# Performance work log

Measured on AMD Instinct MI355X. Metric: run time of the kernel, lower is better.

## Reference

```python
import jax, jax.numpy as jnp
import numpy as np


def setup_inputs() -> dict:
    key = jax.random.key(0)
    kq, kk, kv = jax.random.split(key, 3)
    B, M, QT, KVT, H = 2, 16, 2048, 2048, 128
    q = jax.random.normal(kq, (B, M, QT, H), dtype=jnp.float32)
    k = jax.random.normal(kk, (B, M, KVT, H), dtype=jnp.float32)
    v = jax.random.normal(kv, (B, M, KVT, H), dtype=jnp.float32)
    return {"q": q, "k": k, "v": v}


def reference(q, k, v):
    # QKBmm: broadcast-multiply + sum == einsum contraction over H.
    # NOTE: original module applies NO 1/sqrt(H) scaling.
    score = jnp.einsum("bmqh,bmkh->bmqk", q, k)  # [B,M,QT,KVT]
    score = jax.nn.softmax(score, axis=-1)
    # SVBmm: broadcast-multiply + sum over KVT.
    out = jnp.einsum("bmqk,bmkh->bmqh", score, v)  # [B,M,QT,H]
    return out
```

## Files before the change

### kernel.cpp

```cpp
#include <hip/hip_runtime.h>
#include <hip/hip_bf16.h>
#include <math.h>


#define HD     128
#define QTL    2048
#define KVTL   2048
#define NHEAD  32
#define KVBLK  64
#define NKT    (KVTL / KVBLK)
#define QBLKB  128
#define TILE_BYTES 32768
#define WS_NEEDED ((size_t)NHEAD * NKT * TILE_BYTES)

using f32x4  = __attribute__((ext_vector_type(4))) float;
using f32x16 = __attribute__((ext_vector_type(16))) float;
using f16x8  = __attribute__((ext_vector_type(8))) _Float16;
using f16x2  = __attribute__((ext_vector_type(2))) _Float16;
using i32x2  = __attribute__((ext_vector_type(2))) int;
using i32x4  = __attribute__((ext_vector_type(4))) int;
using bf16x8 = __attribute__((ext_vector_type(8))) __bf16;
using bf16x4 = __attribute__((ext_vector_type(4))) __bf16;

#define NK_CHUNK (NHEAD * NKT * 64 * 16)
#define NV_CHUNK (NHEAD * NKT * 8 * 128)

__global__ __launch_bounds__(256) void sdpa_prep(const float* __restrict__ kg,
                                                 const float* __restrict__ vg,
                                                 char* __restrict__ ws)
{
    const int idx = blockIdx.x * 256 + threadIdx.x;
    if (idx < NK_CHUNK) {
        const int s    = idx & 15;
        const int r    = (idx >> 4) & 63;
        const int kt   = (idx >> 10) & 31;
        const int head = idx >> 15;
        const int c    = s ^ (r & 15);
        const float* src = kg + ((size_t)head * KVTL + kt * 64 + r) * HD + c * 8;
        float4 a = *(const float4*)src;
        float4 b = *(const float4*)(src + 4);
        f16x8 h8;
        h8[0] = (_Float16)a.x; h8[1] = (_Float16)a.y;
        h8[2] = (_Float16)a.z; h8[3] = (_Float16)a.w;
        h8[4] = (_Float16)b.x; h8[5] = (_Float16)b.y;
        h8[6] = (_Float16)b.z; h8[7] = (_Float16)b.w;
        char* base = ws + (size_t)(head * NKT + kt) * TILE_BYTES;
        *(f16x8*)(base + r * 256 + s * 16) = h8;
    } else if (idx < NK_CHUNK + NV_CHUNK) {
        const int j    = idx - NK_CHUNK;
        const int h    = j & 127;
        const int c    = (j >> 7) & 7;
        const int kt   = (j >> 10) & 31;
        const int head = j >> 15;
        const int rr   = h & 63;
        const int u    = h >> 6;
        const int s    = (u * 8 + c) ^ (rr & 15);
        const float* src = vg + ((size_t)head * KVTL + kt * 64 + c * 8) * HD + h;
        f16x8 o;
        #pragma unroll
        for (int i = 0; i < 8; ++i)
            o[i] = (_Float16)src[(size_t)i * HD];
        char* base = ws + (size_t)(head * NKT + kt) * TILE_BYTES;
        *(f16x8*)(base + 16384 + rr * 256 + s * 16) = o;
    }
}

__device__ __forceinline__ void stage_tile(const char* __restrict__ g,
                                           char* lds, int t)
{
    #pragma unroll
    for (int j = 0; j < 8; ++j) {
        __builtin_amdgcn_global_load_lds(
            (const __attribute__((address_space(1))) void*)(g + j * 4096 + t * 16),
            (__attribute__((address_space(3))) void*)(lds + j * 4096 + t * 16),
            16, 0, 0);
    }
}

__global__ __launch_bounds__(256, 2) void sdpa_fwd(const float* __restrict__ qg,
                                                   const char* __restrict__ ws,
                                                   float* __restrict__ og)
{
    const int head  = blockIdx.y;
    const int qblk  = blockIdx.x * QBLKB;
    const float* qh = qg + (size_t)head * QTL * HD;
    const char*  wh = ws + (size_t)head * NKT * TILE_BYTES;

    const int t  = threadIdx.x;
    const int wv = t >> 6;
    const int l  = t & 63;
    const int lq = l & 31;
    const int hi = l >> 5;
    const int lm = l & 15;

    __shared__ __align__(16) char arena[65536];

    f16x8 qf[8];
    {
        const float* qrow = qh + (size_t)(qblk + wv * 32 + lq) * HD;
        #pragma unroll
        for (int hs = 0; hs < 8; ++hs) {
            float4 a = *(const float4*)(qrow + hs * 16 + hi * 8);
            float4 b = *(const float4*)(qrow + hs * 16 + hi * 8 + 4);
            f16x8 f;
            f[0] = (_Float16)a.x; f[1] = (_Float16)a.y;
            f[2] = (_Float16)a.z; f[3] = (_Float16)a.w;
            f[4] = (_Float16)b.x; f[5] = (_Float16)b.y;
            f[6] = (_Float16)b.z; f[7] = (_Float16)b.w;
            qf[hs] = f;
        }
    }

    f32x16 acc_o[4];
    #pragma unroll
    for (int ht = 0; ht < 4; ++ht)
        #pragma unroll
        for (int r = 0; r < 16; ++r) acc_o[ht][r] = 0.f;

    float m = -INFINITY, ln = 0.f;
    const float LOG2E = 1.4426950408889634f;

    stage_tile(wh, arena, t);
    __syncthreads();

    for (int kt = 0; kt < NKT; ++kt) {
        const int cur = kt & 1;
        char* base = arena + cur * 32768;
        if (kt + 1 < NKT)
            stage_tile(wh + (size_t)(kt + 1) * TILE_BYTES, arena + (cur ^ 1) * 32768, t);

        f32x16 acc_s[2];
        #pragma unroll
        for (int kk = 0; kk < 2; ++kk) {
            f32x16 acc;
            #pragma unroll
            for (int r = 0; r < 16; ++r) acc[r] = 0.f;
            #pragma unroll
            for (int hs = 0; hs < 8; ++hs) {
                const int off = (kk * 32 + lq) * 256 + (((hs * 2 + hi) ^ lm) * 16);
                f16x8 kf = *(const f16x8*)(base + off);
                acc = __builtin_amdgcn_mfma_f32_32x32x16_f16(kf, qf[hs], acc, 0, 0, 0);
            }
            acc_s[kk] = acc;
        }

        float pmax = -INFINITY;
        #pragma unroll
        for (int kk = 0; kk < 2; ++kk)
            #pragma unroll
            for (int r = 0; r < 16; ++r) pmax = fmaxf(pmax, acc_s[kk][r]);
        pmax = fmaxf(pmax, __shfl_xor(pmax, 32));

        if (!__all(pmax <= m + 8.0f)) {
            const float mnew = fmaxf(m, pmax);
            const float sc   = exp2f((m - mnew) * LOG2E);
            m = mnew; ln *= sc;
            #pragma unroll
            for (int ht = 0; ht < 4; ++ht)
                #pragma unroll
                for (int r = 0; r < 16; ++r) acc_o[ht][r] *= sc;
        }

        i32x4 fr[4];
        #pragma unroll
        for (int kk = 0; kk < 2; ++kk) {
            float p[16];
            float ps = 0.f;
            #pragma unroll
            for (int r = 0; r < 16; ++r) {
                p[r] = exp2f((acc_s[kk][r] - m) * LOG2E);
                ps += p[r];
            }
            ln += ps;
            int t01 = __builtin_bit_cast(int, __builtin_amdgcn_cvt_pkrtz(p[0],  p[1]));
            int t23 = __builtin_bit_cast(int, __builtin_amdgcn_cvt_pkrtz(p[2],  p[3]));
            int t45 = __builtin_bit_cast(int, __builtin_amdgcn_cvt_pkrtz(p[4],  p[5]));
            int t67 = __builtin_bit_cast(int, __builtin_amdgcn_cvt_pkrtz(p[6],  p[7]));
            int t89 = __builtin_bit_cast(int, __builtin_amdgcn_cvt_pkrtz(p[8],  p[9]));
            int tAB = __builtin_bit_cast(int, __builtin_amdgcn_cvt_pkrtz(p[10], p[11]));
            int tCD = __builtin_bit_cast(int, __builtin_amdgcn_cvt_pkrtz(p[12], p[13]));
            int tEF = __builtin_bit_cast(int, __builtin_amdgcn_cvt_pkrtz(p[14], p[15]));
            i32x2 sw;
            sw = __builtin_amdgcn_permlane32_swap(t01, t45, false, false);
            fr[2*kk][0] = sw[0]; fr[2*kk][2] = sw[1];
            sw = __builtin_amdgcn_permlane32_swap(t23, t67, false, false);
            fr[2*kk][1] = sw[0]; fr[2*kk][3] = sw[1];
            sw = __builtin_amdgcn_permlane32_swap(t89, tCD, false, false);
            fr[2*kk+1][0] = sw[0]; fr[2*kk+1][2] = sw[1];
            sw = __builtin_amdgcn_permlane32_swap(tAB, tEF, false, false);
            fr[2*kk+1][1] = sw[0]; fr[2*kk+1][3] = sw[1];
        }

        const char* Vb = base + 16384;
        #pragma unroll
        for (int ht = 0; ht < 4; ++ht) {
            #pragma unroll
            for (int ks = 0; ks < 4; ++ks) {
                const int off = ((ht & 1) * 32 + lq) * 256 +
                                ((((ht >> 1) * 8 + ks * 2 + hi) ^ lm) * 16);
                f16x8 vf = *(const f16x8*)(Vb + off);
                acc_o[ht] = __builtin_amdgcn_mfma_f32_32x32x16_f16(
                    vf, __builtin_bit_cast(f16x8, fr[ks]), acc_o[ht], 0, 0, 0);
            }
        }

        __syncthreads();
    }

    ln += __shfl_xor(ln, 32);
    const float inv = 1.f / ln;

    __syncthreads();
    const int qloc = wv * 32 + lq;
    #pragma unroll
    for (int ht = 0; ht < 4; ++ht) {
        #pragma unroll
        for (int r = 0; r < 4; ++r) {
            f32x4 v;
            v[0] = acc_o[ht][4*r+0] * inv;
            v[1] = acc_o[ht][4*r+1] * inv;
            v[2] = acc_o[ht][4*r+2] * inv;
            v[3] = acc_o[ht][4*r+3] * inv;
            const int slot = ht * 8 + 2 * r + hi;
            *(f32x4*)(arena + qloc * 512 + ((slot ^ lq) * 16)) = v;
        }
    }
    __syncthreads();
    {
        float* ob = og + (size_t)(head * QTL + qblk) * HD;
        #pragma unroll
        for (int j = 0; j < 16; ++j) {
            const int n  = j * 256 + t;
            const int qr = n >> 5;
            const int sl = n & 31;
            f32x4 v = *(const f32x4*)(arena + qr * 512 + ((sl ^ (qr & 31)) * 16));
            *(f32x4*)(ob + (size_t)qr * HD + sl * 4) = v;
        }
    }
}

__global__ __launch_bounds__(256) void sdpa_fwd_v1(const float* __restrict__ qg,
                                                   const float* __restrict__ kg,
                                                   const float* __restrict__ vg,
                                                   float* __restrict__ og)
{
    const int head  = blockIdx.y;
    const int qbase = blockIdx.x * 64;
    const float* qh = qg + (size_t)head * QTL * HD;
    const float* kh = kg + (size_t)head * KVTL * HD;
    const float* vh = vg + (size_t)head * KVTL * HD;
    float*       oh = og + (size_t)head * QTL * HD;

    const int t  = threadIdx.x;
    const int wv = t >> 6;
    const int l  = t & 63;
    const int lr = l & 15;
    const int lg = l >> 4;

    __shared__ __bf16 Kth[32][HD + 8];
    __shared__ __bf16 Ktl[32][HD + 8];
    __shared__ __bf16 Vt[HD][32 + 8];
    __shared__ __bf16 Pw[4][16][32 + 8];

    bf16x8 qfh[4], qfl[4];
    {
        const float* qrow = qh + (size_t)(qbase + wv * 16 + lr) * HD;
        #pragma unroll
        for (int ks = 0; ks < 4; ++ks) {
            bf16x8 fh, fl;
            #pragma unroll
            for (int i = 0; i < 8; ++i) {
                float x = qrow[ks * 32 + lg * 8 + i];
                __bf16 h = (__bf16)x;
                fh[i] = h;
                fl[i] = (__bf16)(x - (float)h);
            }
            qfh[ks] = fh; qfl[ks] = fl;
        }
    }

    f32x4 acc_o[8];
    #pragma unroll
    for (int h8 = 0; h8 < 8; ++h8) acc_o[h8] = (f32x4){0.f, 0.f, 0.f, 0.f};
    float mrow[4], lrow[4];
    #pragma unroll
    for (int r = 0; r < 4; ++r) { mrow[r] = -INFINITY; lrow[r] = 0.f; }
    const float LOG2E = 1.4426950408889634f;

    for (int kt = 0; kt < 64; ++kt) {
        const float* kbase = kh + (size_t)kt * 32 * HD;
        const float* vbase = vh + (size_t)kt * 32 * HD;
        __syncthreads();
        #pragma unroll
        for (int j = 0; j < 4; ++j) {
            const int e   = (j * 256 + t) * 4;
            const int row = e >> 7;
            const int col = e & 127;
            float4 f = *(const float4*)(kbase + e);
            bf16x4 h4, l4;
            h4[0] = (__bf16)f.x; l4[0] = (__bf16)(f.x - (float)h4[0]);
            h4[1] = (__bf16)f.y; l4[1] = (__bf16)(f.y - (float)h4[1]);
            h4[2] = (__bf16)f.z; l4[2] = (__bf16)(f.z - (float)h4[2]);
            h4[3] = (__bf16)f.w; l4[3] = (__bf16)(f.w - (float)h4[3]);
            *(bf16x4*)&Kth[row][col] = h4;
            *(bf16x4*)&Ktl[row][col] = l4;
        }
        #pragma unroll
        for (int j = 0; j < 4; ++j) {
            const int n     = t & 127;
            const int strip = (t >> 7) + 2 * j;
            bf16x4 b4;
            #pragma unroll
            for (int i = 0; i < 4; ++i)
                b4[i] = (__bf16)vbase[(size_t)(4 * strip + i) * HD + n];
            *(bf16x4*)&Vt[n][4 * strip] = b4;
        }
        __syncthreads();

        f32x4 acc_s[2];
        #pragma unroll
        for (int nt = 0; nt < 2; ++nt) {
            acc_s[nt] = (f32x4){0.f, 0.f, 0.f, 0.f};
            #pragma unroll
            for (int ks = 0; ks < 4; ++ks) {
                bf16x8 kh8 = *(const bf16x8*)&Kth[nt * 16 + lr][ks * 32 + lg * 8];
                bf16x8 kl8 = *(const bf16x8*)&Ktl[nt * 16 + lr][ks * 32 + lg * 8];
                acc_s[nt] = __builtin_amdgcn_mfma_f32_16x16x32_bf16(qfh[ks], kh8, acc_s[nt], 0, 0, 0);
                acc_s[nt] = __builtin_amdgcn_mfma_f32_16x16x32_bf16(qfl[ks], kh8, acc_s[nt], 0, 0, 0);
                acc_s[nt] = __builtin_amdgcn_mfma_f32_16x16x32_bf16(qfh[ks], kl8, acc_s[nt], 0, 0, 0);
            }
        }
        float p[2][4];
        #pragma unroll
        for (int r = 0; r < 4; ++r) {
            float vm = fmaxf(acc_s[0][r], acc_s[1][r]);
            vm = fmaxf(vm, __shfl_xor(vm, 1));
            vm = fmaxf(vm, __shfl_xor(vm, 2));
            vm = fmaxf(vm, __shfl_xor(vm, 4));
            vm = fmaxf(vm, __shfl_xor(vm, 8));
            const float mnew  = fmaxf(mrow[r], vm);
            const float scale = exp2f((mrow[r] - mnew) * LOG2E);
            mrow[r] = mnew;
            float ps = 0.f;
            #pragma unroll
            for (int nt = 0; nt < 2; ++nt) {
                float pe = exp2f((acc_s[nt][r] - mnew) * LOG2E);
                p[nt][r] = pe; ps += pe;
            }
            lrow[r] = lrow[r] * scale + ps;
            #pragma unroll
            for (int h8 = 0; h8 < 8; ++h8) acc_o[h8][r] *= scale;
        }
        #pragma unroll
        for (int nt = 0; nt < 2; ++nt)
            #pragma unroll
            for (int r = 0; r < 4; ++r)
                Pw[wv][lg * 4 + r][nt * 16 + lr] = (__bf16)p[nt][r];
        bf16x8 pf = *(const bf16x8*)&Pw[wv][lr][lg * 8];
        #pragma unroll
        for (int h8 = 0; h8 < 8; ++h8) {
            bf16x8 vf = *(const bf16x8*)&Vt[h8 * 16 + lr][lg * 8];
            acc_o[h8] = __builtin_amdgcn_mfma_f32_16x16x32_bf16(pf, vf, acc_o[h8], 0, 0, 0);
        }
    }
    float invl[4];
    #pragma unroll
    for (int r = 0; r < 4; ++r) {
        float s = lrow[r];
        s += __shfl_xor(s, 1);
        s += __shfl_xor(s, 2);
        s += __shfl_xor(s, 4);
        s += __shfl_xor(s, 8);
        invl[r] = 1.f / s;
    }
    float* ob = oh + (size_t)(qbase + wv * 16) * HD;
    #pragma unroll
    for (int h8 = 0; h8 < 8; ++h8)
        #pragma unroll
        for (int r = 0; r < 4; ++r)
            ob[(size_t)(lg * 4 + r) * HD + h8 * 16 + lr] = acc_o[h8][r] * invl[r];
}

extern "C" void kernel_launch(void* const* d_in, const int* in_sizes, int n_in,
                              void* d_out, int out_size, void* d_ws, size_t ws_size,
                              hipStream_t stream) {
    const float* q = (const float*)d_in[0];
    const float* k = (const float*)d_in[1];
    const float* v = (const float*)d_in[2];
    float* out = (float*)d_out;

    if (ws_size >= WS_NEEDED) {
        char* ws = (char*)d_ws;
        const int total_chunks = NK_CHUNK + NV_CHUNK;
        sdpa_prep<<<total_chunks / 256, 256, 0, stream>>>(k, v, ws);
        dim3 grid(QTL / QBLKB, NHEAD, 1);
        sdpa_fwd<<<grid, dim3(256, 1, 1), 0, stream>>>(q, ws, out);
    } else {
        dim3 grid(QTL / 64, NHEAD, 1);
        sdpa_fwd_v1<<<grid, dim3(256, 1, 1), 0, stream>>>(q, k, v, out);
    }
}
```

Measured before the change: 119.7 us.

## Process two 32-row query tiles per wave to reuse K/V LDS fragments

Each wave now owns 64 query rows split into two 32-row tiles (A and B). Every K and V fragment read from LDS feeds two MFMAs instead of one, which halves LDS reads per unit of math and doubles the query block to 256. The cost is roughly double the accumulator and Q registers, so occupancy drops to one block per CU and the grid shrinks to half as many blocks. The MFMA phases are also wrapped in s_setprio, and the output write-back runs in two passes.

```diff
diff --git a/kernel.cpp b/kernel.cpp
--- a/kernel.cpp
+++ b/kernel.cpp
@@ -9,14 +9,13 @@
 #define NHEAD  32
 #define KVBLK  64
 #define NKT    (KVTL / KVBLK)
-#define QBLKB  128
+#define QBLKB  256
 #define TILE_BYTES 32768
 #define WS_NEEDED ((size_t)NHEAD * NKT * TILE_BYTES)
 
 using f32x4  = __attribute__((ext_vector_type(4))) float;
 using f32x16 = __attribute__((ext_vector_type(16))) float;
 using f16x8  = __attribute__((ext_vector_type(8))) _Float16;
-using f16x2  = __attribute__((ext_vector_type(2))) _Float16;
 using i32x2  = __attribute__((ext_vector_type(2))) int;
 using i32x4  = __attribute__((ext_vector_type(4))) int;
 using bf16x8 = __attribute__((ext_vector_type(8))) __bf16;
@@ -77,7 +76,7 @@
     }
 }
 
-__global__ __launch_bounds__(256, 2) void sdpa_fwd(const float* __restrict__ qg,
+__global__ __launch_bounds__(256, 1) void sdpa_fwd(const float* __restrict__ qg,
                                                    const char* __restrict__ ws,
                                                    float* __restrict__ og)
 {
@@ -95,29 +94,37 @@
 
     __shared__ __align__(16) char arena[65536];
 
-    f16x8 qf[8];
+    f16x8 qfA[8], qfB[8];
     {
-        const float* qrow = qh + (size_t)(qblk + wv * 32 + lq) * HD;
+        const float* qrA = qh + (size_t)(qblk + wv * 64 + lq) * HD;
+        const float* qrB = qrA + 32 * HD;
         #pragma unroll
         for (int hs = 0; hs < 8; ++hs) {
-            float4 a = *(const float4*)(qrow + hs * 16 + hi * 8);
-            float4 b = *(const float4*)(qrow + hs * 16 + hi * 8 + 4);
+            float4 a = *(const float4*)(qrA + hs * 16 + hi * 8);
+            float4 b = *(const float4*)(qrA + hs * 16 + hi * 8 + 4);
             f16x8 f;
             f[0] = (_Float16)a.x; f[1] = (_Float16)a.y;
             f[2] = (_Float16)a.z; f[3] = (_Float16)a.w;
             f[4] = (_Float16)b.x; f[5] = (_Float16)b.y;
             f[6] = (_Float16)b.z; f[7] = (_Float16)b.w;
-            qf[hs] = f;
-        }
-    }
-
-    f32x16 acc_o[4];
+            qfA[hs] = f;
+            a = *(const float4*)(qrB + hs * 16 + hi * 8);
+            b = *(const float4*)(qrB + hs * 16 + hi * 8 + 4);
+            f[0] = (_Float16)a.x; f[1] = (_Float16)a.y;
+            f[2] = (_Float16)a.z; f[3] = (_Float16)a.w;
+            f[4] = (_Float16)b.x; f[5] = (_Float16)b.y;
+            f[6] = (_Float16)b.z; f[7] = (_Float16)b.w;
+            qfB[hs] = f;
+        }
+    }
+
+    f32x16 accA[4], accB[4];
     #pragma unroll
     for (int ht = 0; ht < 4; ++ht)
         #pragma unroll
-        for (int r = 0; r < 16; ++r) acc_o[ht][r] = 0.f;
-
-    float m = -INFINITY, ln = 0.f;
+        for (int r = 0; r < 16; ++r) { accA[ht][r] = 0.f; accB[ht][r] = 0.f; }
+
+    float mA = -INFINITY, mB = -INFINITY, lnA = 0.f, lnB = 0.f;
     const float LOG2E = 1.4426950408889634f;
 
     stage_tile(wh, arena, t);
@@ -129,69 +136,88 @@
         if (kt + 1 < NKT)
             stage_tile(wh + (size_t)(kt + 1) * TILE_BYTES, arena + (cur ^ 1) * 32768, t);
 
-        f32x16 acc_s[2];
-        #pragma unroll
-        for (int kk = 0; kk < 2; ++kk) {
-            f32x16 acc;
-            #pragma unroll
-            for (int r = 0; r < 16; ++r) acc[r] = 0.f;
-            #pragma unroll
-            for (int hs = 0; hs < 8; ++hs) {
-                const int off = (kk * 32 + lq) * 256 + (((hs * 2 + hi) ^ lm) * 16);
-                f16x8 kf = *(const f16x8*)(base + off);
-                acc = __builtin_amdgcn_mfma_f32_32x32x16_f16(kf, qf[hs], acc, 0, 0, 0);
-            }
-            acc_s[kk] = acc;
-        }
-
-        float pmax = -INFINITY;
-        #pragma unroll
-        for (int kk = 0; kk < 2; ++kk)
-            #pragma unroll
-            for (int r = 0; r < 16; ++r) pmax = fmaxf(pmax, acc_s[kk][r]);
-        pmax = fmaxf(pmax, __shfl_xor(pmax, 32));
-
-        if (!__all(pmax <= m + 8.0f)) {
-            const float mnew = fmaxf(m, pmax);
-            const float sc   = exp2f((m - mnew) * LOG2E);
-            m = mnew; ln *= sc;
+        f32x16 sA0, sA1, sB0, sB1;
+        #pragma unroll
+        for (int r = 0; r < 16; ++r) { sA0[r] = 0.f; sA1[r] = 0.f; sB0[r] = 0.f; sB1[r] = 0.f; }
+        __builtin_amdgcn_s_setprio(1);
+        #pragma unroll
+        for (int hs = 0; hs < 8; ++hs) {
+            const int soff = (((hs * 2 + hi) ^ lm) * 16);
+            f16x8 kf0 = *(const f16x8*)(base + lq * 256 + soff);
+            f16x8 kf1 = *(const f16x8*)(base + (32 + lq) * 256 + soff);
+            sA0 = __builtin_amdgcn_mfma_f32_32x32x16_f16(kf0, qfA[hs], sA0, 0, 0, 0);
+            sB0 = __builtin_amdgcn_mfma_f32_32x32x16_f16(kf0, qfB[hs], sB0, 0, 0, 0);
+            sA1 = __builtin_amdgcn_mfma_f32_32x32x16_f16(kf1, qfA[hs], sA1, 0, 0, 0);
+            sB1 = __builtin_amdgcn_mfma_f32_32x32x16_f16(kf1, qfB[hs], sB1, 0, 0, 0);
+        }
+        __builtin_amdgcn_s_setprio(0);
+
+        float pmA0 = -INFINITY, pmA1 = -INFINITY, pmB0 = -INFINITY, pmB1 = -INFINITY;
+        #pragma unroll
+        for (int r = 0; r < 16; r += 2) {
+            pmA0 = fmaxf(pmA0, fmaxf(sA0[r], sA0[r + 1]));
+            pmA1 = fmaxf(pmA1, fmaxf(sA1[r], sA1[r + 1]));
+            pmB0 = fmaxf(pmB0, fmaxf(sB0[r], sB0[r + 1]));
+            pmB1 = fmaxf(pmB1, fmaxf(sB1[r], sB1[r + 1]));
+        }
+        float pmA = fmaxf(pmA0, pmA1);
+        float pmB = fmaxf(pmB0, pmB1);
+        pmA = fmaxf(pmA, __shfl_xor(pmA, 32));
+        pmB = fmaxf(pmB, __shfl_xor(pmB, 32));
+
+        const bool need = (pmA > mA + 8.0f) || (pmB > mB + 8.0f);
+        if (__any(need)) {
+            const float mAn = fmaxf(mA, pmA);
+            const float mBn = fmaxf(mB, pmB);
+            const float scA = exp2f((mA - mAn) * LOG2E);
+            const float scB = exp2f((mB - mBn) * LOG2E);
+            mA = mAn; mB = mBn; lnA *= scA; lnB *= scB;
             #pragma unroll
             for (int ht = 0; ht < 4; ++ht)
                 #pragma unroll
-                for (int r = 0; r < 16; ++r) acc_o[ht][r] *= sc;
-        }
-
-        i32x4 fr[4];
-        #pragma unroll
-        for (int kk = 0; kk < 2; ++kk) {
-            float p[16];
-            float ps = 0.f;
-            #pragma unroll
-            for (int r = 0; r < 16; ++r) {
-                p[r] = exp2f((acc_s[kk][r] - m) * LOG2E);
-                ps += p[r];
-            }
-            ln += ps;
-            int t01 = __builtin_bit_cast(int, __builtin_amdgcn_cvt_pkrtz(p[0],  p[1]));
-            int t23 = __builtin_bit_cast(int, __builtin_amdgcn_cvt_pkrtz(p[2],  p[3]));
-            int t45 = __builtin_bit_cast(int, __builtin_amdgcn_cvt_pkrtz(p[4],  p[5]));
-            int t67 = __builtin_bit_cast(int, __builtin_amdgcn_cvt_pkrtz(p[6],  p[7]));
-            int t89 = __builtin_bit_cast(int, __builtin_amdgcn_cvt_pkrtz(p[8],  p[9]));
-            int tAB = __builtin_bit_cast(int, __builtin_amdgcn_cvt_pkrtz(p[10], p[11]));
-            int tCD = __builtin_bit_cast(int, __builtin_amdgcn_cvt_pkrtz(p[12], p[13]));
-            int tEF = __builtin_bit_cast(int, __builtin_amdgcn_cvt_pkrtz(p[14], p[15]));
-            i32x2 sw;
-            sw = __builtin_amdgcn_permlane32_swap(t01, t45, false, false);
-            fr[2*kk][0] = sw[0]; fr[2*kk][2] = sw[1];
-            sw = __builtin_amdgcn_permlane32_swap(t23, t67, false, false);
-            fr[2*kk][1] = sw[0]; fr[2*kk][3] = sw[1];
-            sw = __builtin_amdgcn_permlane32_swap(t89, tCD, false, false);
-            fr[2*kk+1][0] = sw[0]; fr[2*kk+1][2] = sw[1];
-            sw = __builtin_amdgcn_permlane32_swap(tAB, tEF, false, false);
-            fr[2*kk+1][1] = sw[0]; fr[2*kk+1][3] = sw[1];
+                for (int r = 0; r < 16; ++r) { accA[ht][r] *= scA; accB[ht][r] *= scB; }
+        }
+
+        i32x4 frA[4], frB[4];
+        #pragma unroll
+        for (int f = 0; f < 2; ++f) {
+            const float mf = f ? mB : mA;
+            #pragma unroll
+            for (int kk = 0; kk < 2; ++kk) {
+                const f32x16& s = f ? (kk ? sB1 : sB0) : (kk ? sA1 : sA0);
+                i32x4* fr = f ? frB : frA;
+                float p[16];
+                float a0 = 0.f, a1 = 0.f, a2 = 0.f, a3 = 0.f;
+                #pragma unroll
+                for (int r = 0; r < 16; r += 4) {
+                    p[r + 0] = exp2f((s[r + 0] - mf) * LOG2E); a0 += p[r + 0];
+                    p[r + 1] = exp2f((s[r + 1] - mf) * LOG2E); a1 += p[r + 1];
+                    p[r + 2] = exp2f((s[r + 2] - mf) * LOG2E); a2 += p[r + 2];
+                    p[r + 3] = exp2f((s[r + 3] - mf) * LOG2E); a3 += p[r + 3];
+                }
+                if (f) lnB += (a0 + a1) + (a2 + a3); else lnA += (a0 + a1) + (a2 + a3);
+                int t01 = __builtin_bit_cast(int, __builtin_amdgcn_cvt_pkrtz(p[0],  p[1]));
+                int t23 = __builtin_bit_cast(int, __builtin_amdgcn_cvt_pkrtz(p[2],  p[3]));
+                int t45 = __builtin_bit_cast(int, __builtin_amdgcn_cvt_pkrtz(p[4],  p[5]));
+                int t67 = __builtin_bit_cast(int, __builtin_amdgcn_cvt_pkrtz(p[6],  p[7]));
+                int t89 = __builtin_bit_cast(int, __builtin_amdgcn_cvt_pkrtz(p[8],  p[9]));
+                int tAB = __builtin_bit_cast(int, __builtin_amdgcn_cvt_pkrtz(p[10], p[11]));
+                int tCD = __builtin_bit_cast(int, __builtin_amdgcn_cvt_pkrtz(p[12], p[13]));
+                int tEF = __builtin_bit_cast(int, __builtin_amdgcn_cvt_pkrtz(p[14], p[15]));
+                i32x2 sw;
+                sw = __builtin_amdgcn_permlane32_swap(t01, t45, false, false);
+                fr[2*kk][0] = sw[0]; fr[2*kk][2] = sw[1];
+                sw = __builtin_amdgcn_permlane32_swap(t23, t67, false, false);
+                fr[2*kk][1] = sw[0]; fr[2*kk][3] = sw[1];
+                sw = __builtin_amdgcn_permlane32_swap(t89, tCD, false, false);
+                fr[2*kk+1][0] = sw[0]; fr[2*kk+1][2] = sw[1];
+                sw = __builtin_amdgcn_permlane32_swap(tAB, tEF, false, false);
+                fr[2*kk+1][1] = sw[0]; fr[2*kk+1][3] = sw[1];
+            }
         }
 
         const char* Vb = base + 16384;
+        __builtin_amdgcn_s_setprio(1);
         #pragma unroll
         for (int ht = 0; ht < 4; ++ht) {
             #pragma unroll
@@ -199,42 +225,50 @@
                 const int off = ((ht & 1) * 32 + lq) * 256 +
                                 ((((ht >> 1) * 8 + ks * 2 + hi) ^ lm) * 16);
                 f16x8 vf = *(const f16x8*)(Vb + off);
-                acc_o[ht] = __builtin_amdgcn_mfma_f32_32x32x16_f16(
-                    vf, __builtin_bit_cast(f16x8, fr[ks]), acc_o[ht], 0, 0, 0);
-            }
-        }
+                accA[ht] = __builtin_amdgcn_mfma_f32_32x32x16_f16(
+                    vf, __builtin_bit_cast(f16x8, frA[ks]), accA[ht], 0, 0, 0);
+                accB[ht] = __builtin_amdgcn_mfma_f32_32x32x16_f16(
+                    vf, __builtin_bit_cast(f16x8, frB[ks]), accB[ht], 0, 0, 0);
+            }
+        }
+        __builtin_amdgcn_s_setprio(0);
 
         __syncthreads();
     }
 
-    ln += __shfl_xor(ln, 32);
-    const float inv = 1.f / ln;
-
-    __syncthreads();
-    const int qloc = wv * 32 + lq;
-    #pragma unroll
-    for (int ht = 0; ht < 4; ++ht) {
-        #pragma unroll
-        for (int r = 0; r < 4; ++r) {
-            f32x4 v;
-            v[0] = acc_o[ht][4*r+0] * inv;
-            v[1] = acc_o[ht][4*r+1] * inv;
-            v[2] = acc_o[ht][4*r+2] * inv;
-            v[3] = acc_o[ht][4*r+3] * inv;
-            const int slot = ht * 8 + 2 * r + hi;
-            *(f32x4*)(arena + qloc * 512 + ((slot ^ lq) * 16)) = v;
-        }
-    }
-    __syncthreads();
-    {
-        float* ob = og + (size_t)(head * QTL + qblk) * HD;
+    lnA += __shfl_xor(lnA, 32);
+    lnB += __shfl_xor(lnB, 32);
+    const float invA = 1.f / lnA;
+    const float invB = 1.f / lnB;
+
+    #pragma unroll
+    for (int f = 0; f < 2; ++f) {
+        const f32x16* acc = f ? accB : accA;
+        const float  inv  = f ? invB : invA;
+        __syncthreads();
+        const int lrow = wv * 32 + lq;
+        #pragma unroll
+        for (int ht = 0; ht < 4; ++ht) {
+            #pragma unroll
+            for (int r = 0; r < 4; ++r) {
+                f32x4 v;
+                v[0] = acc[ht][4*r+0] * inv;
+                v[1] = acc[ht][4*r+1] * inv;
+                v[2] = acc[ht][4*r+2] * inv;
+                v[3] = acc[ht][4*r+3] * inv;
+                const int slot = ht * 8 + 2 * r + hi;
+                *(f32x4*)(arena + lrow * 512 + ((slot ^ lq) * 16)) = v;
+            }
+        }
+        __syncthreads();
         #pragma unroll
         for (int j = 0; j < 16; ++j) {
             const int n  = j * 256 + t;
             const int qr = n >> 5;
             const int sl = n & 31;
             f32x4 v = *(const f32x4*)(arena + qr * 512 + ((sl ^ (qr & 31)) * 16));
-            *(f32x4*)(ob + (size_t)qr * HD + sl * 4) = v;
+            const int grow = qblk + (qr >> 5) * 64 + f * 32 + (qr & 31);
+            *(f32x4*)(og + ((size_t)head * QTL + grow) * HD + sl * 4) = v;
         }
     }
 }
```

Measured after the change: 153.4 us. 28.1% more time.
